# Optimization experiments

Measured on AMD Instinct MI355X. Metric: run time of the kernel, lower is better.

Reference implementation:

```python
import jax, jax.numpy as jnp
import numpy as np

B, M, D = 8, 8192, 1024   # batch, tokens, latent_dim
N, P = 128, 1             # num_experts, slots_per_expert
F = 4096                  # expert_dim


def setup_inputs() -> dict:
    key = jax.random.key(0)
    k_x, k_phi, k_w1, k_b1, k_w2, k_b2 = jax.random.split(key, 6)
    x = jax.random.normal(k_x, (B, M, D), dtype=jnp.float32)
    # phi initialized as randn(d, n, p) / sqrt(d) in the original
    phi = jax.random.normal(k_phi, (D, N, P), dtype=jnp.float32) / (D ** 0.5)
    # Single shared expert MLP (original aliases one nn.Sequential across all experts)
    W1 = jax.random.normal(k_w1, (D, F), dtype=jnp.float32) / (D ** 0.5)
    b1 = jax.random.normal(k_b1, (F,), dtype=jnp.float32) * 0.01
    W2 = jax.random.normal(k_w2, (F, D), dtype=jnp.float32) / (F ** 0.5)
    b2 = jax.random.normal(k_b2, (D,), dtype=jnp.float32) * 0.01
    return {"x": x, "phi": phi, "W1": W1, "b1": b1, "W2": W2, "b2": b2}


def reference(x, phi, W1, b1, W2, b2):
    # dispatch / combine logits: [b, m, n, p]
    logits = jnp.einsum('bmd,dnp->bmnp', x, phi)
    d = jax.nn.softmax(logits, axis=1)                      # softmax over tokens m
    b_, m_, n_, p_ = logits.shape
    c = jax.nn.softmax(logits.reshape(b_, m_, n_ * p_), axis=-1).reshape(b_, m_, n_, p_)
    # slot inputs: [b, n, p, d]
    x_i = jnp.einsum('bmd,bmnp->bnpd', x, d)
    # shared expert MLP (torch GELU default = exact erf)
    h = jax.nn.gelu(jnp.einsum('bnpd,df->bnpf', x_i, W1) + b1, approximate=False)
    y_i = jnp.einsum('bnpf,fd->bnpd', h, W2) + b2
    # combine: [b, m, d]
    y = jnp.einsum('bnpd,bmnp->bmd', y_i, c)
    return y
```

## Files before the change

### kernel.cpp

```cpp
#include <hip/hip_runtime.h>
#include <math.h>

#define Bq 8
#define Mq 8192
#define Dq 1024
#define Nq 128
#define Fq 4096

typedef __bf16 bf16x8 __attribute__((ext_vector_type(8)));
typedef float f32x4 __attribute__((ext_vector_type(4)));
union P4 { __bf16 h[4]; unsigned long long u; };

__device__ __forceinline__ int swz128(int row, int bcol) {
  return row * 128 + (bcol ^ ((row & 7) << 4));
}
__device__ __forceinline__ int swz256(int row, int bcol) {
  return row * 256 + (bcol ^ ((row & 7) << 4));
}

__global__ __launch_bounds__(256) void wconv(const float* __restrict__ src,
                                             unsigned long long* __restrict__ dst, long n4)
{
  long i = (long)blockIdx.x * 256 + threadIdx.x;
  if (i >= n4) return;
  float4 v = ((const float4*)src)[i];
  P4 p; p.h[0] = (__bf16)v.x; p.h[1] = (__bf16)v.y; p.h[2] = (__bf16)v.z; p.h[3] = (__bf16)v.w;
  dst[i] = p.u;
}

__global__ __launch_bounds__(256) void logits_mfma(
    const float* __restrict__ x, const float* __restrict__ phi,
    __bf16* __restrict__ ebuf, __bf16* __restrict__ cbuf)
{
  __shared__ __align__(16) char sA[16384];
  __shared__ __align__(16) char sP[16384];
  int mt = blockIdx.x, b = blockIdx.y;
  int m0 = mt * 128;
  int t = threadIdx.x;
  int col = t & 127, half = t >> 7;
  int arow = t >> 4, ac4 = t & 15;
  int w = t >> 6, l = t & 63, la = l & 15, lb = l >> 4;

  f32x4 zero = {0.f, 0.f, 0.f, 0.f};
  f32x4 acc[2][8];
  for (int i = 0; i < 2; ++i) for (int j = 0; j < 8; ++j) acc[i][j] = zero;

  for (int k0 = 0; k0 < Dq; k0 += 64) {
    #pragma unroll
    for (int i = 0; i < 8; ++i) {
      int row = arow + 16 * i;
      float4 v = *(const float4*)(x + ((long)b * Mq + m0 + row) * Dq + k0 + ac4 * 4);
      P4 p;
      p.h[0] = (__bf16)v.x; p.h[1] = (__bf16)v.y;
      p.h[2] = (__bf16)v.z; p.h[3] = (__bf16)v.w;
      *(unsigned long long*)(sA + swz128(row, 8 * ac4)) = p.u;
    }
    {
      const float* Pp = phi + (long)(k0 + half * 32) * Nq + col;
      #pragma unroll
      for (int i = 0; i < 32; i += 4) {
        float a0 = Pp[(i + 0) * Nq], a1 = Pp[(i + 1) * Nq];
        float a2 = Pp[(i + 2) * Nq], a3 = Pp[(i + 3) * Nq];
        P4 p;
        p.h[0] = (__bf16)a0; p.h[1] = (__bf16)a1;
        p.h[2] = (__bf16)a2; p.h[3] = (__bf16)a3;
        *(unsigned long long*)(sP + swz128(col, 2 * (half * 32 + i))) = p.u;
      }
    }
    __syncthreads();
    #pragma unroll
    for (int sub = 0; sub < 2; ++sub) {
      int mbyte = sub * 64 + lb * 16;
      bf16x8 af0 = *(const bf16x8*)(sA + swz128(w * 32 + la, mbyte));
      bf16x8 af1 = *(const bf16x8*)(sA + swz128(w * 32 + 16 + la, mbyte));
      bf16x8 bv[8];
      #pragma unroll
      for (int j = 0; j < 8; ++j)
        bv[j] = *(const bf16x8*)(sP + swz128(j * 16 + la, mbyte));
      #pragma unroll
      for (int j = 0; j < 8; ++j) {
        acc[0][j] = __builtin_amdgcn_mfma_f32_16x16x32_bf16(af0, bv[j], acc[0][j], 0, 0, 0);
        acc[1][j] = __builtin_amdgcn_mfma_f32_16x16x32_bf16(af1, bv[j], acc[1][j], 0, 0, 0);
      }
    }
    __syncthreads();
  }
  float inv[2][4];
  #pragma unroll
  for (int i = 0; i < 2; ++i)
    #pragma unroll
    for (int r = 0; r < 4; ++r) {
      float s = 0.f;
      #pragma unroll
      for (int j = 0; j < 8; ++j) s += __expf(acc[i][j][r]);
      s += __shfl_xor(s, 1); s += __shfl_xor(s, 2);
      s += __shfl_xor(s, 4); s += __shfl_xor(s, 8);
      inv[i][r] = 1.0f / s;
    }
  __bf16* Eb = ebuf + ((long)b * Mq + m0) * Nq;
  __bf16* Cb = cbuf + ((long)b * Mq + m0) * Nq;
  #pragma unroll
  for (int i = 0; i < 2; ++i)
    #pragma unroll
    for (int j = 0; j < 8; ++j)
      #pragma unroll
      for (int r = 0; r < 4; ++r) {
        int row = w * 32 + i * 16 + lb * 4 + r;
        int colg = j * 16 + la;
        float e = __expf(acc[i][j][r]);
        Eb[(long)row * Nq + colg] = (__bf16)e;
        Cb[(long)row * Nq + colg] = (__bf16)(e * inv[i][r]);
      }
}

__global__ __launch_bounds__(256) void colsum_part(const __bf16* __restrict__ ebuf,
                                                   float* __restrict__ psum)
{
  __shared__ float red[256];
  int chunk = blockIdx.x, b = blockIdx.y;
  int t = threadIdx.x, n = t & 127, half = t >> 7;
  const __bf16* Ep = ebuf + ((long)b * Mq + chunk * 256 + half * 128) * Nq + n;
  float s = 0.f;
  for (int i = 0; i < 128; ++i) s += (float)Ep[(long)i * Nq];
  red[t] = s;
  __syncthreads();
  if (t < 128) psum[((long)chunk * Bq + b) * Nq + n] = red[t] + red[t + 128];
}

__global__ void colsum_fin(const float* __restrict__ psum, float* __restrict__ cinv)
{
  int b = blockIdx.x, n = threadIdx.x;
  float s = 0.f;
  for (int k = 0; k < 32; ++k) s += psum[((long)k * Bq + b) * Nq + n];
  cinv[b * Nq + n] = 1.0f / s;
}

__global__ __launch_bounds__(256) void xi_mfma(
    const __bf16* __restrict__ ebuf, const float* __restrict__ x,
    float* __restrict__ part)
{
  __shared__ __align__(16) char sD[16384];
  __shared__ __align__(16) char sX[8192];
  int dt = blockIdx.x, kc = blockIdx.y, b = blockIdx.z;
  int d0 = dt * 64;
  int t = threadIdx.x;
  int col = t & 127, half = t >> 7;
  int cd = t & 63, grp = t >> 6;
  const __bf16* Ep0 = ebuf + ((long)b * Mq + (long)kc * 2048 + half * 32) * Nq + col;
  const float* Xp0 = x + ((long)b * Mq + (long)kc * 2048 + grp * 16) * Dq + d0 + cd;
  int w = t >> 6, l = t & 63, la = l & 15, lb = l >> 4;

  f32x4 zero = {0.f, 0.f, 0.f, 0.f};
  f32x4 acc[2][4];
  for (int i = 0; i < 2; ++i) for (int j = 0; j < 4; ++j) acc[i][j] = zero;

  for (int it = 0; it < 32; ++it) {
    const __bf16* Ep = Ep0 + (long)it * 64 * Nq;
    const float* Xp = Xp0 + (long)it * 64 * Dq;
    #pragma unroll
    for (int i = 0; i < 32; i += 4) {
      P4 p;
      p.h[0] = Ep[(long)(i + 0) * Nq]; p.h[1] = Ep[(long)(i + 1) * Nq];
      p.h[2] = Ep[(long)(i + 2) * Nq]; p.h[3] = Ep[(long)(i + 3) * Nq];
      *(unsigned long long*)(sD + swz128(col, 2 * (half * 32 + i))) = p.u;
    }
    #pragma unroll
    for (int i = 0; i < 16; i += 4) {
      float b0 = Xp[(long)(i + 0) * Dq], b1 = Xp[(long)(i + 1) * Dq];
      float b2 = Xp[(long)(i + 2) * Dq], b3 = Xp[(long)(i + 3) * Dq];
      P4 q;
      q.h[0] = (__bf16)b0; q.h[1] = (__bf16)b1;
      q.h[2] = (__bf16)b2; q.h[3] = (__bf16)b3;
      *(unsigned long long*)(sX + swz128(cd, 2 * (grp * 16 + i))) = q.u;
    }
    __syncthreads();
    #pragma unroll
    for (int sub = 0; sub < 2; ++sub) {
      int mbyte = sub * 64 + lb * 16;
      bf16x8 af0 = *(const bf16x8*)(sD + swz128(w * 32 + la, mbyte));
      bf16x8 af1 = *(const bf16x8*)(sD + swz128(w * 32 + 16 + la, mbyte));
      bf16x8 bv[4];
      #pragma unroll
      for (int j = 0; j < 4; ++j)
        bv[j] = *(const bf16x8*)(sX + swz128(j * 16 + la, mbyte));
      #pragma unroll
      for (int j = 0; j < 4; ++j) {
        acc[0][j] = __builtin_amdgcn_mfma_f32_16x16x32_bf16(af0, bv[j], acc[0][j], 0, 0, 0);
        acc[1][j] = __builtin_amdgcn_mfma_f32_16x16x32_bf16(af1, bv[j], acc[1][j], 0, 0, 0);
      }
    }
    __syncthreads();
  }
  float* P = part + ((long)kc * Bq + b) * Nq * (long)Dq + d0;
  #pragma unroll
  for (int i = 0; i < 2; ++i)
    #pragma unroll
    for (int j = 0; j < 4; ++j)
      #pragma unroll
      for (int r = 0; r < 4; ++r)
        P[(long)(w * 32 + i * 16 + lb * 4 + r) * Dq + j * 16 + la] = acc[i][j][r];
}

__global__ __launch_bounds__(256) void xi_reduce(const float* __restrict__ part,
    const float* __restrict__ cinv, __bf16* __restrict__ xib)
{
  long idx = (long)blockIdx.x * 256 + threadIdx.x;
  int row = (int)(idx >> 10);
  float civ = cinv[row];
  float s = part[idx] + part[idx + 1048576] + part[idx + 2097152] + part[idx + 3145728];
  xib[idx] = (__bf16)(s * civ);
}

template<int EPI, typename OT>
__global__ __launch_bounds__(256) void gemm_bf16(const __bf16* __restrict__ A,
    const __bf16* __restrict__ Bw, const float* __restrict__ bias,
    OT* __restrict__ C, int lda, int ldb, int ldc, int kLen, long strideCz)
{
  __shared__ __align__(16) char sA[16384];
  __shared__ __align__(16) char sB[16384];
  int m0 = blockIdx.x * 128, n0 = blockIdx.y * 128;
  int kbase = blockIdx.z * kLen;
  C += (long)blockIdx.z * strideCz;
  int t = threadIdx.x;
  int col = t & 127, half = t >> 7;
  int w = t >> 6, l = t & 63, la = l & 15, lb = l >> 4;

  f32x4 zero = {0.f, 0.f, 0.f, 0.f};
  f32x4 acc[2][8];
  for (int i = 0; i < 2; ++i) for (int j = 0; j < 8; ++j) acc[i][j] = zero;

  for (int kt = 0; kt < kLen; kt += 64) {
    int kp = kbase + kt;
    #pragma unroll
    for (int s = 0; s < 4; ++s) {
      int idx = t + 256 * s;
      int row = idx >> 3, c8 = idx & 7;
      *(int4*)(sA + swz128(row, c8 * 16)) =
          *(const int4*)(A + (long)(m0 + row) * lda + kp + c8 * 8);
    }
    {
      const __bf16* Bp = Bw + (long)(kp + half * 32) * ldb + n0 + col;
      #pragma unroll
      for (int i = 0; i < 32; i += 4) {
        P4 p;
        p.h[0] = Bp[(long)(i + 0) * ldb]; p.h[1] = Bp[(long)(i + 1) * ldb];
        p.h[2] = Bp[(long)(i + 2) * ldb]; p.h[3] = Bp[(long)(i + 3) * ldb];
        *(unsigned long long*)(sB + swz128(col, 2 * (half * 32 + i))) = p.u;
      }
    }
    __syncthreads();
    #pragma unroll
    for (int sub = 0; sub < 2; ++sub) {
      int mbyte = sub * 64 + lb * 16;
      bf16x8 af0 = *(const bf16x8*)(sA + swz128(w * 32 + la, mbyte));
      bf16x8 af1 = *(const bf16x8*)(sA + swz128(w * 32 + 16 + la, mbyte));
      bf16x8 bv[8];
      #pragma unroll
      for (int j = 0; j < 8; ++j)
        bv[j] = *(const bf16x8*)(sB + swz128(j * 16 + la, mbyte));
      #pragma unroll
      for (int j = 0; j < 8; ++j) {
        acc[0][j] = __builtin_amdgcn_mfma_f32_16x16x32_bf16(af0, bv[j], acc[0][j], 0, 0, 0);
        acc[1][j] = __builtin_amdgcn_mfma_f32_16x16x32_bf16(af1, bv[j], acc[1][j], 0, 0, 0);
      }
    }
    __syncthreads();
  }
  #pragma unroll
  for (int i = 0; i < 2; ++i)
    #pragma unroll
    for (int j = 0; j < 8; ++j)
      #pragma unroll
      for (int r = 0; r < 4; ++r) {
        int row = m0 + w * 32 + i * 16 + lb * 4 + r;
        int colg = n0 + j * 16 + la;
        float v = acc[i][j][r];
        if (EPI == 2) {
          v += bias[colg];
          v = 0.5f * v * (1.0f + erff(v * 0.70710678118654752f));
        }
        C[(long)row * ldc + colg] = (OT)v;
      }
}

__global__ __launch_bounds__(256) void g2_reduce(const float* __restrict__ part,
    const float* __restrict__ b2, __bf16* __restrict__ yiT)
{
  long idx = (long)blockIdx.x * 256 + threadIdx.x;
  int row = (int)(idx >> 10);
  int d = (int)(idx & 1023);
  float s = part[idx] + part[idx + 1048576] + part[idx + 2097152] + part[idx + 3145728] + b2[d];
  int b = row >> 7, n = row & 127;
  yiT[((long)b * Dq + d) * Nq + n] = (__bf16)s;
}

__global__ __launch_bounds__(256) void combine_mfma(const __bf16* __restrict__ cbuf,
    const __bf16* __restrict__ yiT, float* __restrict__ y)
{
  __shared__ __align__(16) char sC[32768];
  __shared__ __align__(16) char sY[32768];
  int mt = blockIdx.x, dt = blockIdx.y, b = blockIdx.z;
  int m0 = mt * 128, d0 = dt * 128;
  int t = threadIdx.x;
  #pragma unroll
  for (int s = 0; s < 8; ++s) {
    int idx = t + 256 * s;
    int row = idx >> 4, c16 = idx & 15;
    *(int4*)(sC + swz256(row, c16 * 16)) =
        *(const int4*)(cbuf + ((long)b * Mq + m0 + row) * Nq + c16 * 8);
    *(int4*)(sY + swz256(row, c16 * 16)) =
        *(const int4*)(yiT + ((long)b * Dq + d0 + row) * Nq + c16 * 8);
  }
  __syncthreads();
  int w = t >> 6, l = t & 63, la = l & 15, lb = l >> 4;
  f32x4 zero = {0.f, 0.f, 0.f, 0.f};
  f32x4 acc[2][8];
  for (int i = 0; i < 2; ++i) for (int j = 0; j < 8; ++j) acc[i][j] = zero;
  #pragma unroll
  for (int sub = 0; sub < 4; ++sub) {
    int mbyte = sub * 64 + lb * 16;
    bf16x8 af0 = *(const bf16x8*)(sC + swz256(w * 32 + la, mbyte));
    bf16x8 af1 = *(const bf16x8*)(sC + swz256(w * 32 + 16 + la, mbyte));
    bf16x8 bv[8];
    #pragma unroll
    for (int j = 0; j < 8; ++j)
      bv[j] = *(const bf16x8*)(sY + swz256(j * 16 + la, mbyte));
    #pragma unroll
    for (int j = 0; j < 8; ++j) {
      acc[0][j] = __builtin_amdgcn_mfma_f32_16x16x32_bf16(af0, bv[j], acc[0][j], 0, 0, 0);
      acc[1][j] = __builtin_amdgcn_mfma_f32_16x16x32_bf16(af1, bv[j], acc[1][j], 0, 0, 0);
    }
  }
  float* Y = y + ((long)b * Mq + m0) * Dq + d0;
  #pragma unroll
  for (int i = 0; i < 2; ++i)
    #pragma unroll
    for (int j = 0; j < 8; ++j)
      #pragma unroll
      for (int r = 0; r < 4; ++r)
        Y[(long)(w * 32 + i * 16 + lb * 4 + r) * Dq + j * 16 + la] = acc[i][j][r];
}

extern "C" void kernel_launch(void* const* d_in, const int* in_sizes, int n_in,
                              void* d_out, int out_size, void* d_ws, size_t ws_size,
                              hipStream_t stream) {
  const float* x   = (const float*)d_in[0];
  const float* phi = (const float*)d_in[1];
  const float* W1  = (const float*)d_in[2];
  const float* b1  = (const float*)d_in[3];
  const float* W2  = (const float*)d_in[4];
  const float* b2  = (const float*)d_in[5];
  float* y = (float*)d_out;

  char* W = (char*)d_ws;
  __bf16* cbuf  = (__bf16*)W;
  __bf16* ebuf  = (__bf16*)(W + 16777216);
  __bf16* h     = ebuf;
  float*  xipart= (float*)(W + 33554432);
  float*  g2part= xipart;
  __bf16* W1b   = (__bf16*)(W + 50331648);
  __bf16* W2b   = (__bf16*)(W + 58720256);
  __bf16* xib   = (__bf16*)(W + 67108864);
  __bf16* yiT   = (__bf16*)(W + 69206016);
  float*  psum  = (float*)(W + 71303168);
  float*  cinv  = (float*)(W + 71434240);

  wconv<<<4096, 256, 0, stream>>>(W1, (unsigned long long*)W1b, 1048576);
  wconv<<<4096, 256, 0, stream>>>(W2, (unsigned long long*)W2b, 1048576);
  logits_mfma<<<dim3(Mq / 128, Bq), 256, 0, stream>>>(x, phi, ebuf, cbuf);
  colsum_part<<<dim3(32, Bq), 256, 0, stream>>>(ebuf, psum);
  colsum_fin<<<Bq, 128, 0, stream>>>(psum, cinv);
  xi_mfma<<<dim3(Dq / 64, 4, Bq), 256, 0, stream>>>(ebuf, x, xipart);
  xi_reduce<<<4096, 256, 0, stream>>>(xipart, cinv, xib);
  gemm_bf16<2, __bf16><<<dim3(8, 32, 1), 256, 0, stream>>>(
      xib, W1b, b1, h, Dq, Fq, Fq, 1024, 0L);
  gemm_bf16<0, float><<<dim3(8, 8, 4), 256, 0, stream>>>(
      h, W2b, nullptr, g2part, Fq, Dq, Dq, 1024, 1048576L);
  g2_reduce<<<4096, 256, 0, stream>>>(g2part, b2, yiT);
  combine_mfma<<<dim3(Mq / 128, Dq / 128, Bq), 256, 0, stream>>>(cbuf, yiT, y);
}
```

Before: 442.4 us.

## Transpose exp-logits buffer, register-prefetch xi GEMM, fp16 partials, fused column sums

The logits kernel now writes the unnormalised exponentials transposed (expert-major, token-contiguous). This lets the column-sum kernel read rows with vectorised 16-byte loads in a single pass and lets xi_mfma load its A operand with contiguous int4 loads instead of strided scalar bf16 gathers. xi_mfma is split over 8 K-chunks instead of 4 and double-buffers through registers, prefetching the next tile during the MFMAs. Its partials are stored as fp16, which halves the partial traffic but adds rounding error and a risk of overflow. The reduction kernel is vectorised to process 8 elements per thread.

```diff
diff --git a/kernel.cpp b/kernel.cpp
--- a/kernel.cpp
+++ b/kernel.cpp
@@ -10,6 +10,8 @@
 typedef __bf16 bf16x8 __attribute__((ext_vector_type(8)));
 typedef float f32x4 __attribute__((ext_vector_type(4)));
 union P4 { __bf16 h[4]; unsigned long long u; };
+union H8 { int4 v; _Float16 h[8]; };
+union B8 { int4 v; __bf16 h[8]; };
 
 __device__ __forceinline__ int swz128(int row, int bcol) {
   return row * 128 + (bcol ^ ((row & 7) << 4));
@@ -30,7 +32,7 @@
 
 __global__ __launch_bounds__(256) void logits_mfma(
     const float* __restrict__ x, const float* __restrict__ phi,
-    __bf16* __restrict__ ebuf, __bf16* __restrict__ cbuf)
+    __bf16* __restrict__ eT, __bf16* __restrict__ cbuf)
 {
   __shared__ __align__(16) char sA[16384];
   __shared__ __align__(16) char sP[16384];
@@ -97,83 +99,91 @@
       s += __shfl_xor(s, 4); s += __shfl_xor(s, 8);
       inv[i][r] = 1.0f / s;
     }
-  __bf16* Eb = ebuf + ((long)b * Mq + m0) * Nq;
   __bf16* Cb = cbuf + ((long)b * Mq + m0) * Nq;
+  __bf16* Eb = eT + (long)b * Nq * Mq + m0;
   #pragma unroll
   for (int i = 0; i < 2; ++i)
     #pragma unroll
-    for (int j = 0; j < 8; ++j)
+    for (int j = 0; j < 8; ++j) {
+      P4 p;
       #pragma unroll
       for (int r = 0; r < 4; ++r) {
         int row = w * 32 + i * 16 + lb * 4 + r;
-        int colg = j * 16 + la;
         float e = __expf(acc[i][j][r]);
-        Eb[(long)row * Nq + colg] = (__bf16)e;
-        Cb[(long)row * Nq + colg] = (__bf16)(e * inv[i][r]);
-      }
-}
-
-__global__ __launch_bounds__(256) void colsum_part(const __bf16* __restrict__ ebuf,
-                                                   float* __restrict__ psum)
-{
-  __shared__ float red[256];
-  int chunk = blockIdx.x, b = blockIdx.y;
-  int t = threadIdx.x, n = t & 127, half = t >> 7;
-  const __bf16* Ep = ebuf + ((long)b * Mq + chunk * 256 + half * 128) * Nq + n;
+        p.h[r] = (__bf16)e;
+        Cb[(long)row * Nq + j * 16 + la] = (__bf16)(e * inv[i][r]);
+      }
+      *(unsigned long long*)(Eb + (long)(j * 16 + la) * Mq + w * 32 + i * 16 + lb * 4) = p.u;
+    }
+}
+
+__global__ __launch_bounds__(256) void colsum_rows(const __bf16* __restrict__ eT,
+                                                   float* __restrict__ cinv)
+{
+  __shared__ float red[4];
+  int r = blockIdx.x;
+  int t = threadIdx.x;
+  const __bf16* p = eT + (long)r * Mq;
   float s = 0.f;
-  for (int i = 0; i < 128; ++i) s += (float)Ep[(long)i * Nq];
-  red[t] = s;
+  #pragma unroll
+  for (int k = 0; k < 4; ++k) {
+    B8 v; v.v = *(const int4*)(p + t * 8 + k * 2048);
+    #pragma unroll
+    for (int e = 0; e < 8; ++e) s += (float)v.h[e];
+  }
+  #pragma unroll
+  for (int off = 32; off >= 1; off >>= 1) s += __shfl_down(s, off);
+  if ((t & 63) == 0) red[t >> 6] = s;
   __syncthreads();
-  if (t < 128) psum[((long)chunk * Bq + b) * Nq + n] = red[t] + red[t + 128];
-}
-
-__global__ void colsum_fin(const float* __restrict__ psum, float* __restrict__ cinv)
-{
-  int b = blockIdx.x, n = threadIdx.x;
-  float s = 0.f;
-  for (int k = 0; k < 32; ++k) s += psum[((long)k * Bq + b) * Nq + n];
-  cinv[b * Nq + n] = 1.0f / s;
+  if (t == 0) cinv[r] = 1.0f / (red[0] + red[1] + red[2] + red[3]);
 }
 
 __global__ __launch_bounds__(256) void xi_mfma(
-    const __bf16* __restrict__ ebuf, const float* __restrict__ x,
-    float* __restrict__ part)
+    const __bf16* __restrict__ eT, const float* __restrict__ x,
+    _Float16* __restrict__ part)
 {
   __shared__ __align__(16) char sD[16384];
   __shared__ __align__(16) char sX[8192];
   int dt = blockIdx.x, kc = blockIdx.y, b = blockIdx.z;
   int d0 = dt * 64;
   int t = threadIdx.x;
-  int col = t & 127, half = t >> 7;
+  int arow = t >> 1, ahalf = t & 1;
+  const __bf16* Ep0 = eT + ((long)b * Nq + arow) * Mq + (long)kc * 1024 + ahalf * 32;
   int cd = t & 63, grp = t >> 6;
-  const __bf16* Ep0 = ebuf + ((long)b * Mq + (long)kc * 2048 + half * 32) * Nq + col;
-  const float* Xp0 = x + ((long)b * Mq + (long)kc * 2048 + grp * 16) * Dq + d0 + cd;
+  const float* Xp0 = x + ((long)b * Mq + (long)kc * 1024 + grp * 16) * Dq + d0 + cd;
   int w = t >> 6, l = t & 63, la = l & 15, lb = l >> 4;
 
   f32x4 zero = {0.f, 0.f, 0.f, 0.f};
   f32x4 acc[2][4];
   for (int i = 0; i < 2; ++i) for (int j = 0; j < 4; ++j) acc[i][j] = zero;
 
-  for (int it = 0; it < 32; ++it) {
-    const __bf16* Ep = Ep0 + (long)it * 64 * Nq;
-    const float* Xp = Xp0 + (long)it * 64 * Dq;
-    #pragma unroll
-    for (int i = 0; i < 32; i += 4) {
-      P4 p;
-      p.h[0] = Ep[(long)(i + 0) * Nq]; p.h[1] = Ep[(long)(i + 1) * Nq];
-      p.h[2] = Ep[(long)(i + 2) * Nq]; p.h[3] = Ep[(long)(i + 3) * Nq];
-      *(unsigned long long*)(sD + swz128(col, 2 * (half * 32 + i))) = p.u;
-    }
-    #pragma unroll
-    for (int i = 0; i < 16; i += 4) {
-      float b0 = Xp[(long)(i + 0) * Dq], b1 = Xp[(long)(i + 1) * Dq];
-      float b2 = Xp[(long)(i + 2) * Dq], b3 = Xp[(long)(i + 3) * Dq];
-      P4 q;
-      q.h[0] = (__bf16)b0; q.h[1] = (__bf16)b1;
-      q.h[2] = (__bf16)b2; q.h[3] = (__bf16)b3;
-      *(unsigned long long*)(sX + swz128(cd, 2 * (grp * 16 + i))) = q.u;
-    }
-    __syncthreads();
+  int4 ar[4];
+  float br[16];
+  #pragma unroll
+  for (int q = 0; q < 4; ++q) ar[q] = *(const int4*)(Ep0 + q * 8);
+  #pragma unroll
+  for (int i = 0; i < 16; ++i) br[i] = Xp0[(long)i * Dq];
+  #pragma unroll
+  for (int q = 0; q < 4; ++q)
+    *(int4*)(sD + swz128(arow, ahalf * 64 + q * 16)) = ar[q];
+  #pragma unroll
+  for (int q = 0; q < 4; ++q) {
+    P4 p;
+    p.h[0] = (__bf16)br[4 * q + 0]; p.h[1] = (__bf16)br[4 * q + 1];
+    p.h[2] = (__bf16)br[4 * q + 2]; p.h[3] = (__bf16)br[4 * q + 3];
+    *(unsigned long long*)(sX + swz128(cd, grp * 32 + q * 8)) = p.u;
+  }
+
+  for (int it = 0; it < 16; ++it) {
+    __syncthreads();
+    if (it < 15) {
+      #pragma unroll
+      for (int q = 0; q < 4; ++q)
+        ar[q] = *(const int4*)(Ep0 + (it + 1) * 64 + q * 8);
+      #pragma unroll
+      for (int i = 0; i < 16; ++i)
+        br[i] = Xp0[((long)(it + 1) * 64 + i) * Dq];
+    }
     #pragma unroll
     for (int sub = 0; sub < 2; ++sub) {
       int mbyte = sub * 64 + lb * 16;
@@ -190,25 +200,46 @@
       }
     }
     __syncthreads();
-  }
-  float* P = part + ((long)kc * Bq + b) * Nq * (long)Dq + d0;
+    if (it < 15) {
+      #pragma unroll
+      for (int q = 0; q < 4; ++q)
+        *(int4*)(sD + swz128(arow, ahalf * 64 + q * 16)) = ar[q];
+      #pragma unroll
+      for (int q = 0; q < 4; ++q) {
+        P4 p;
+        p.h[0] = (__bf16)br[4 * q + 0]; p.h[1] = (__bf16)br[4 * q + 1];
+        p.h[2] = (__bf16)br[4 * q + 2]; p.h[3] = (__bf16)br[4 * q + 3];
+        *(unsigned long long*)(sX + swz128(cd, grp * 32 + q * 8)) = p.u;
+      }
+    }
+  }
+  _Float16* P = part + ((long)kc * Bq + b) * (long)Nq * Dq + d0;
   #pragma unroll
   for (int i = 0; i < 2; ++i)
     #pragma unroll
     for (int j = 0; j < 4; ++j)
       #pragma unroll
       for (int r = 0; r < 4; ++r)
-        P[(long)(w * 32 + i * 16 + lb * 4 + r) * Dq + j * 16 + la] = acc[i][j][r];
-}
-
-__global__ __launch_bounds__(256) void xi_reduce(const float* __restrict__ part,
+        P[(long)(w * 32 + i * 16 + lb * 4 + r) * Dq + j * 16 + la] = (_Float16)acc[i][j][r];
+}
+
+__global__ __launch_bounds__(256) void xi_reduce(const _Float16* __restrict__ part,
     const float* __restrict__ cinv, __bf16* __restrict__ xib)
 {
-  long idx = (long)blockIdx.x * 256 + threadIdx.x;
-  int row = (int)(idx >> 10);
+  long base = ((long)blockIdx.x * 256 + threadIdx.x) * 8;
+  int row = (int)(base >> 10);
   float civ = cinv[row];
-  float s = part[idx] + part[idx + 1048576] + part[idx + 2097152] + part[idx + 3145728];
-  xib[idx] = (__bf16)(s * civ);
+  float s[8] = {};
+  #pragma unroll
+  for (int k = 0; k < 8; ++k) {
+    H8 v; v.v = *(const int4*)(part + (long)k * 1048576 + base);
+    #pragma unroll
+    for (int e = 0; e < 8; ++e) s[e] += (float)v.h[e];
+  }
+  B8 o;
+  #pragma unroll
+  for (int e = 0; e < 8; ++e) o.h[e] = (__bf16)(s[e] * civ);
+  *(int4*)(xib + base) = o.v;
 }
 
 template<int EPI, typename OT>
@@ -353,25 +384,23 @@
   float* y = (float*)d_out;
 
   char* W = (char*)d_ws;
-  __bf16* cbuf  = (__bf16*)W;
-  __bf16* ebuf  = (__bf16*)(W + 16777216);
-  __bf16* h     = ebuf;
-  float*  xipart= (float*)(W + 33554432);
-  float*  g2part= xipart;
-  __bf16* W1b   = (__bf16*)(W + 50331648);
-  __bf16* W2b   = (__bf16*)(W + 58720256);
-  __bf16* xib   = (__bf16*)(W + 67108864);
-  __bf16* yiT   = (__bf16*)(W + 69206016);
-  float*  psum  = (float*)(W + 71303168);
-  float*  cinv  = (float*)(W + 71434240);
+  __bf16*   cbuf   = (__bf16*)W;
+  __bf16*   eT     = (__bf16*)(W + 16777216);
+  __bf16*   h      = eT;
+  _Float16* part   = (_Float16*)(W + 33554432);
+  float*    g2part = (float*)(W + 33554432);
+  __bf16*   W1b    = (__bf16*)(W + 50331648);
+  __bf16*   W2b    = (__bf16*)(W + 58720256);
+  __bf16*   xib    = (__bf16*)(W + 67108864);
+  __bf16*   yiT    = (__bf16*)(W + 69206016);
+  float*    cinv   = (float*)(W + 71303168);
 
   wconv<<<4096, 256, 0, stream>>>(W1, (unsigned long long*)W1b, 1048576);
   wconv<<<4096, 256, 0, stream>>>(W2, (unsigned long long*)W2b, 1048576);
-  logits_mfma<<<dim3(Mq / 128, Bq), 256, 0, stream>>>(x, phi, ebuf, cbuf);
-  colsum_part<<<dim3(32, Bq), 256, 0, stream>>>(ebuf, psum);
-  colsum_fin<<<Bq, 128, 0, stream>>>(psum, cinv);
-  xi_mfma<<<dim3(Dq / 64, 4, Bq), 256, 0, stream>>>(ebuf, x, xipart);
-  xi_reduce<<<4096, 256, 0, stream>>>(xipart, cinv, xib);
+  logits_mfma<<<dim3(Mq / 128, Bq), 256, 0, stream>>>(x, phi, eT, cbuf);
+  colsum_rows<<<Bq * Nq, 256, 0, stream>>>(eT, cinv);
+  xi_mfma<<<dim3(Dq / 64, 8, Bq), 256, 0, stream>>>(eT, x, part);
+  xi_reduce<<<512, 256, 0, stream>>>(part, cinv, xib);
   gemm_bf16<2, __bf16><<<dim3(8, 32, 1), 256, 0, stream>>>(
       xib, W1b, b1, h, Dq, Fq, Fq, 1024, 0L);
   gemm_bf16<0, float><<<dim3(8, 8, 4), 256, 0, stream>>>(
```

Result: no change. 440.0 us (-0.5%).
